# Kernel tuning notes

Hardware: AMD Instinct MI355X
Metric: run time of the kernel (lower is better)

## Reference

```python
import jax, jax.numpy as jnp
import numpy as np

DIM = 512
HEADS = 8
DEPTH = DIM // HEADS
DFF = 2048
EPS = 1e-3  # keras BatchNormalization default epsilon


def _dense_params(key, d_in, d_out, bias=True):
    k1, k2 = jax.random.split(key)
    lim = 1.0 / np.sqrt(d_in)
    W = jax.random.uniform(k1, (d_in, d_out), minval=-lim, maxval=lim, dtype=jnp.float32)
    if bias:
        b = jnp.zeros((d_out,), jnp.float32)
        return W, b
    return W


def _bn_params(key, d):
    k1, k2 = jax.random.split(key)
    gamma = 1.0 + 0.1 * jax.random.normal(k1, (d,), jnp.float32)
    beta = 0.1 * jax.random.normal(k2, (d,), jnp.float32)
    mean = 0.05 * jax.random.normal(jax.random.fold_in(key, 7), (d,), jnp.float32)
    var = jnp.ones((d,), jnp.float32)
    return gamma, beta, mean, var


def setup_inputs() -> dict:
    key = jax.random.key(0)
    ks = jax.random.split(key, 20)
    B, S_dec, S_enc = 32, 384, 384
    inp = {
        'enc_output': jax.random.normal(ks[0], (B, S_enc, DIM), jnp.float32),
        'x2': jax.random.normal(ks[1], (B, S_dec, DIM), jnp.float32),
    }
    # mha1 (self-attn) params
    for i, nm in enumerate(['q1', 'k1', 'v1', 'o1']):
        W, b = _dense_params(ks[2 + i], DIM, DIM)
        inp[f'W{nm}'], inp[f'b{nm}'] = W, b
    # mha2 (cross-attn) params
    for i, nm in enumerate(['q2', 'k2', 'v2', 'o2']):
        W, b = _dense_params(ks[6 + i], DIM, DIM)
        inp[f'W{nm}'], inp[f'b{nm}'] = W, b
    # FFN
    inp['Wff1'] = _dense_params(ks[10], DIM, DFF, bias=False)
    inp['Wff2'] = _dense_params(ks[11], DFF, DIM, bias=False)
    # 4 batchnorms
    for i in range(1, 5):
        g, be, m, v = _bn_params(ks[11 + i], DIM)
        inp[f'bn{i}_gamma'], inp[f'bn{i}_beta'] = g, be
        inp[f'bn{i}_mean'], inp[f'bn{i}_var'] = m, v
    return inp


def _split_heads(x):
    B, S, _ = x.shape
    return x.reshape(B, S, HEADS, DEPTH).transpose(0, 2, 1, 3)


def _mha(q_in, k_in, v_in, Wq, bq, Wk, bk, Wv, bv, Wo, bo, causal):
    q = _split_heads(q_in @ Wq + bq)
    k = _split_heads(k_in @ Wk + bk)
    v = _split_heads(v_in @ Wv + bv)
    logits = jnp.einsum('bhqd,bhkd->bhqk', q, k) / jnp.sqrt(jnp.float32(DEPTH))
    if causal:
        Sq, Sk = logits.shape[-2], logits.shape[-1]
        mask = jnp.tril(jnp.ones((Sq, Sk), bool))
        logits = jnp.where(mask, logits, jnp.finfo(logits.dtype).min)
    attn = jax.nn.softmax(logits, axis=-1)
    out = jnp.einsum('bhqk,bhkd->bhqd', attn, v)
    B, _, S, _ = out.shape
    out = out.transpose(0, 2, 1, 3).reshape(B, S, DIM)
    return out @ Wo + bo


def _bn(x, gamma, beta, mean, var):
    return (x - mean) * jax.lax.rsqrt(var + EPS) * gamma + beta


def reference(enc_output, x2,
              Wq1, bq1, Wk1, bk1, Wv1, bv1, Wo1, bo1,
              Wq2, bq2, Wk2, bk2, Wv2, bv2, Wo2, bo2,
              Wff1, Wff2,
              bn1_gamma, bn1_beta, bn1_mean, bn1_var,
              bn2_gamma, bn2_beta, bn2_mean, bn2_var,
              bn3_gamma, bn3_beta, bn3_mean, bn3_var,
              bn4_gamma, bn4_beta, bn4_mean, bn4_var):
    # self-attention with causal mask (dropout = identity)
    x = _mha(x2, x2, x2, Wq1, bq1, Wk1, bk1, Wv1, bv1, Wo1, bo1, causal=True)
    x = x + x2
    xn = _bn(x, bn1_gamma, bn1_beta, bn1_mean, bn1_var)
    y = _bn(enc_output, bn2_gamma, bn2_beta, bn2_mean, bn2_var)
    # cross-attention (no mask); residual adds x2 (as in source)
    x = _mha(xn, y, y, Wq2, bq2, Wk2, bk2, Wv2, bv2, Wo2, bo2, causal=False)
    x = x + x2
    cross_out = x
    x = _bn(x, bn3_gamma, bn3_beta, bn3_mean, bn3_var)
    x = jax.nn.relu(x @ Wff1) @ Wff2
    x = x + cross_out
    x = _bn(x, bn4_gamma, bn4_beta, bn4_mean, bn4_var)
    return x
```

## Files before the change

### kernel.cpp

```cpp
#include <hip/hip_runtime.h>
#include <cstdint>
#include <cstddef>

typedef __bf16 bf16;
typedef __bf16 bf16x8 __attribute__((ext_vector_type(8)));
typedef __bf16 bf16x4 __attribute__((ext_vector_type(4)));
typedef float  f32x4  __attribute__((ext_vector_type(4)));

#define B_   32
#define S_   384
#define D_   512
#define H_   8
#define DH_  64
#define DFF_ 2048
#define NTOK (B_*S_)

__device__ __forceinline__ void gload16(const void* g, void* l){
  __builtin_amdgcn_global_load_lds((__attribute__((address_space(1))) uint32_t*)(g),
                                   (__attribute__((address_space(3))) uint32_t*)(l), 16, 0, 0);
}

struct Ptr8 { const float* s[8]; };
__global__ __launch_bounds__(256) void transpose_w8(Ptr8 ps, bf16* dst){
  __shared__ float t[64][65];
  int w = blockIdx.z;
  const float* src = ps.s[w];
  bf16* d = dst + (size_t)w*512*512;
  int tr = blockIdx.y*64, tc = blockIdx.x*64;
  for (int i=threadIdx.x; i<4096; i+=256){ int r=i>>6, c=i&63; t[r][c] = src[(size_t)(tr+r)*512 + tc+c]; }
  __syncthreads();
  for (int i=threadIdx.x; i<4096; i+=256){ int c=i>>6, r=i&63; d[(size_t)(tc+c)*512 + tr+r] = (bf16)t[r][c]; }
}

__global__ __launch_bounds__(256) void transpose_rc(const float* __restrict__ src, bf16* __restrict__ dst,
                                                    int R, int C){
  __shared__ float t[64][65];
  int tr = blockIdx.y*64, tc = blockIdx.x*64;
  for (int i=threadIdx.x; i<4096; i+=256){ int r=i>>6, c=i&63; t[r][c] = src[(size_t)(tr+r)*C + tc+c]; }
  __syncthreads();
  for (int i=threadIdx.x; i<4096; i+=256){ int c=i>>6, r=i&63; dst[(size_t)(tc+c)*R + tr+r] = (bf16)t[r][c]; }
}

struct Ptr16 { const float* p[16]; };
__global__ __launch_bounds__(512) void bn_prep(Ptr16 q, float* sc, float* sh){
  int i = blockIdx.x;
  int n = threadIdx.x;
  float g = q.p[i*4+0][n];
  float b = q.p[i*4+1][n];
  float m = q.p[i*4+2][n];
  float v = q.p[i*4+3][n];
  float s = g * rsqrtf(v + 1e-3f);
  sc[i*512+n] = s;
  sh[i*512+n] = b - m*s;
}

__global__ __launch_bounds__(256) void cvt2(const float* __restrict__ enc, const float* __restrict__ x2,
                                            const float* __restrict__ sc, const float* __restrict__ sh,
                                            bf16* __restrict__ E2, bf16* __restrict__ X2b){
  size_t e0 = ((size_t)blockIdx.x*256 + threadIdx.x)*4;
  if (blockIdx.y == 0){
    int n0 = (int)(e0 & (D_-1));
    f32x4 xv = *(const f32x4*)(enc + e0);
    bf16x4 ov;
    #pragma unroll
    for (int j=0;j<4;j++) ov[j] = (bf16)(xv[j]*sc[n0+j] + sh[n0+j]);
    *(bf16x4*)(E2 + e0) = ov;
  } else {
    f32x4 xv = *(const f32x4*)(x2 + e0);
    bf16x4 ov;
    #pragma unroll
    for (int j=0;j<4;j++) ov[j] = (bf16)xv[j];
    *(bf16x4*)(X2b + e0) = ov;
  }
}

__global__ __launch_bounds__(256,3) void gemm_bt(
    const bf16* __restrict__ A, const bf16* __restrict__ Wt,
    const float* __restrict__ b0, const float* __restrict__ b1, const float* __restrict__ b2,
    const bf16* __restrict__ residb,
    const float* __restrict__ bsc, const float* __restrict__ bsh,
    bf16* __restrict__ o0, bf16* __restrict__ o1b,
    bf16* __restrict__ vt, int vseg,
    float* __restrict__ of, bf16* __restrict__ pre,
    int M, int N, int K, int relu, int mode)
{
  __shared__ bf16 As[2][64*64];
  __shared__ bf16 Bs[2][128*64];
  int nwg = gridDim.x;
  int cpx = nwg >> 3;
  int bid = blockIdx.x;
  int swz = (bid & 7)*cpx + (bid >> 3);
  int tiles_n = N >> 7;
  int tm = swz / tiles_n, tn = swz - tm*tiles_n;

  int tid = threadIdx.x, wave = tid>>6, lane = tid&63;
  int lhi = lane>>4, llo = lane&15;
  int lrow = lane>>3, lcol = lane&7;
  int wr = wave>>1, wc = wave&1;

  f32x4 acc[2][4];
  #pragma unroll
  for (int i=0;i<2;i++)
    #pragma unroll
    for (int j=0;j<4;j++) acc[i][j] = (f32x4){0.f,0.f,0.f,0.f};

  const bf16* Abase = A  + (size_t)(tm*64)  * K;
  const bf16* Bbase = Wt + (size_t)(tn*128) * K;

  int arow0 = wave*16, brow0 = wave*32;

  auto STAGE = [&](int buf, int kt){
    #pragma unroll
    for (int q=0;q<2;q++){
      int r = arow0 + q*8 + lrow;
      int s = lcol ^ (r&7);
      gload16(Abase + (size_t)r*K + kt + s*8, (char*)&As[buf][0] + wave*2048 + q*1024);
    }
    #pragma unroll
    for (int q=0;q<4;q++){
      int r = brow0 + q*8 + lrow;
      int s = lcol ^ (r&7);
      gload16(Bbase + (size_t)r*K + kt + s*8, (char*)&Bs[buf][0] + wave*4096 + q*1024);
    }
  };

  STAGE(0, 0);
  __syncthreads();
  int nt = K >> 6;
  int cur = 0;
  for (int t=0; t<nt; ++t){
    if (t+1 < nt) STAGE(cur^1, (t+1)<<6);
    #pragma unroll
    for (int ks=0; ks<2; ks++){
      bf16x8 af[2], bfr[4];
      #pragma unroll
      for (int i=0;i<2;i++){
        int row = wr*32 + i*16 + llo;
        int slot = (ks*4 + lhi) ^ (row&7);
        af[i] = *(const bf16x8*)&As[cur][row*64 + slot*8];
      }
      #pragma unroll
      for (int j=0;j<4;j++){
        int row = wc*64 + j*16 + llo;
        int slot = (ks*4 + lhi) ^ (row&7);
        bfr[j] = *(const bf16x8*)&Bs[cur][row*64 + slot*8];
      }
      #pragma unroll
      for (int i=0;i<2;i++)
        #pragma unroll
        for (int j=0;j<4;j++)
          acc[i][j] = __builtin_amdgcn_mfma_f32_16x16x32_bf16(af[i], bfr[j], acc[i][j], 0,0,0);
    }
    __syncthreads();
    cur ^= 1;
  }

  int m0 = tm*64 + wr*32, n0 = tn*128 + wc*64;
  #pragma unroll
  for (int i=0;i<2;i++){
    #pragma unroll
    for (int j=0;j<4;j++){
      int gn = n0 + j*16 + llo;
      float vv[4];
      #pragma unroll
      for (int rr=0;rr<4;rr++){
        int gm = m0 + i*16 + lhi*4 + rr;
        float v = acc[i][j][rr];
        if (b0){
          const float* bp = (gn < 512) ? b0 : ((gn < 1024) ? b1 : b2);
          v += bp[gn & 511];
        }
        if (residb) v += (float)residb[(size_t)gm*N + gn];
        vv[rr] = v;
      }
      int gm0 = m0 + i*16 + lhi*4;
      if (mode == 1){
        int seg = gn >> 9, cn = gn & 511;
        int h = cn >> 6, dd = cn & 63;
        int bb = gm0 / S_, ss0 = gm0 - bb*S_;
        if (seg == vseg){
          bf16x4 v4;
          #pragma unroll
          for (int rr=0;rr<4;rr++) v4[rr] = (bf16)vv[rr];
          *(bf16x4*)&vt[((size_t)(bb*H_ + h)*DH_ + dd)*S_ + ss0] = v4;
        } else {
          bf16* hp = (seg == 0) ? o0 : o1b;
          #pragma unroll
          for (int rr=0;rr<4;rr++)
            hp[(((size_t)(bb*H_ + h))*S_ + ss0 + rr)*DH_ + dd] = (bf16)vv[rr];
        }
      } else {
        #pragma unroll
        for (int rr=0;rr<4;rr++){
          int gm = gm0 + rr;
          float v = vv[rr];
          if (pre)  pre[(size_t)gm*N + gn] = (bf16)v;
          if (bsc)  v = v*bsc[gn & 511] + bsh[gn & 511];
          if (relu) v = fmaxf(v, 0.f);
          if (of) of[(size_t)gm*N + gn] = v;
          else    o0[(size_t)gm*N + gn] = (bf16)v;
        }
      }
    }
  }
}

__global__ __launch_bounds__(256,4) void gemm_bt2(
    const bf16* __restrict__ A, const bf16* __restrict__ Wt,
    const float* __restrict__ b0, const float* __restrict__ b1, const float* __restrict__ b2,
    const bf16* __restrict__ residb,
    bf16* __restrict__ o0, bf16* __restrict__ o1b,
    bf16* __restrict__ vt, int vseg,
    int M, int N, int K, int relu, int mode)
{
  __shared__ bf16 As[2][128*32];
  __shared__ bf16 Bs[2][128*32];
  int nwg = gridDim.x;
  int cpx = nwg >> 3;
  int bid = blockIdx.x;
  int swz = (bid & 7)*cpx + (bid >> 3);
  int tiles_n = N >> 7;
  int tm = swz / tiles_n, tn = swz - tm*tiles_n;

  int tid = threadIdx.x, wave = tid>>6, lane = tid&63;
  int lhi = lane>>4, llo = lane&15;
  int srow = lane>>2, sslot = lane&3;
  int wr = wave>>1, wc = wave&1;

  f32x4 acc[4][4];
  #pragma unroll
  for (int i=0;i<4;i++)
    #pragma unroll
    for (int j=0;j<4;j++) acc[i][j] = (f32x4){0.f,0.f,0.f,0.f};

  const bf16* Abase = A  + (size_t)(tm*128) * K;
  const bf16* Bbase = Wt + (size_t)(tn*128) * K;

  auto STAGE = [&](int buf, int kt){
    #pragma unroll
    for (int q=0;q<2;q++){
      int r = wave*32 + q*16 + srow;
      int s = sslot ^ ((r>>1)&3);
      gload16(Abase + (size_t)r*K + kt + s*8, (char*)&As[buf][0] + wave*2048 + q*1024);
    }
    #pragma unroll
    for (int q=0;q<2;q++){
      int r = wave*32 + q*16 + srow;
      int s = sslot ^ ((r>>1)&3);
      gload16(Bbase + (size_t)r*K + kt + s*8, (char*)&Bs[buf][0] + wave*2048 + q*1024);
    }
  };

  STAGE(0, 0);
  __syncthreads();
  int nt = K >> 5;
  int cur = 0;
  for (int t=0; t<nt; ++t){
    if (t+1 < nt) STAGE(cur^1, (t+1)<<5);
    bf16x8 af[4], bfr[4];
    #pragma unroll
    for (int i=0;i<4;i++){
      int row = wr*64 + i*16 + llo;
      int slot = lhi ^ ((row>>1)&3);
      af[i] = *(const bf16x8*)&As[cur][row*32 + slot*8];
    }
    #pragma unroll
    for (int j=0;j<4;j++){
      int row = wc*64 + j*16 + llo;
      int slot = lhi ^ ((row>>1)&3);
      bfr[j] = *(const bf16x8*)&Bs[cur][row*32 + slot*8];
    }
    #pragma unroll
    for (int i=0;i<4;i++)
      #pragma unroll
      for (int j=0;j<4;j++)
        acc[i][j] = __builtin_amdgcn_mfma_f32_16x16x32_bf16(af[i], bfr[j], acc[i][j], 0,0,0);
    __syncthreads();
    cur ^= 1;
  }

  int m0 = tm*128 + wr*64, n0 = tn*128 + wc*64;
  #pragma unroll
  for (int i=0;i<4;i++){
    #pragma unroll
    for (int j=0;j<4;j++){
      int gn = n0 + j*16 + llo;
      float vv[4];
      #pragma unroll
      for (int rr=0;rr<4;rr++){
        int gm = m0 + i*16 + lhi*4 + rr;
        float v = acc[i][j][rr];
        if (b0){
          const float* bp = (gn < 512) ? b0 : ((gn < 1024) ? b1 : b2);
          v += bp[gn & 511];
        }
        if (residb) v += (float)residb[(size_t)gm*N + gn];
        vv[rr] = v;
      }
      int gm0 = m0 + i*16 + lhi*4;
      if (mode == 1){
        int seg = gn >> 9, cn = gn & 511;
        int h = cn >> 6, dd = cn & 63;
        int bb = gm0 / S_, ss0 = gm0 - bb*S_;
        if (seg == vseg){
          bf16x4 v4;
          #pragma unroll
          for (int rr=0;rr<4;rr++) v4[rr] = (bf16)vv[rr];
          *(bf16x4*)&vt[((size_t)(bb*H_ + h)*DH_ + dd)*S_ + ss0] = v4;
        } else {
          bf16* hp = (seg == 0) ? o0 : o1b;
          #pragma unroll
          for (int rr=0;rr<4;rr++)
            hp[(((size_t)(bb*H_ + h))*S_ + ss0 + rr)*DH_ + dd] = (bf16)vv[rr];
        }
      } else {
        #pragma unroll
        for (int rr=0;rr<4;rr++){
          int gm = gm0 + rr;
          float v = vv[rr];
          if (relu) v = fmaxf(v, 0.f);
          o0[(size_t)gm*N + gn] = (bf16)v;
        }
      }
    }
  }
}

__global__ __launch_bounds__(256,4) void attn(
    const bf16* __restrict__ Q, const bf16* __restrict__ Kx,
    const bf16* __restrict__ Vt, bf16* __restrict__ out, int causal)
{
  __shared__ bf16 Ks[64*64];
  __shared__ bf16 Vs[64*64];
  __shared__ bf16 Ps[4][16*64];
  int bid = blockIdx.x;
  int bh = bid & 255;
  int qb = bid >> 8;
  int b = bh >> 3, h = bh & 7;
  int tid = threadIdx.x, wave = tid>>6, lane = tid&63;
  int lhi = lane>>4, llo = lane&15;
  int l7 = llo & 7;
  const bf16* Qb = Q  + (size_t)bh*S_*DH_;
  const bf16* Kb = Kx + (size_t)bh*S_*DH_;
  const bf16* Vb = Vt + (size_t)bh*DH_*S_;

  bf16x8 qf[2];
  #pragma unroll
  for (int f=0; f<2; f++)
    qf[f] = *(const bf16x8*)&Qb[(size_t)(qb*64 + wave*16 + llo)*DH_ + f*32 + lhi*8];

  f32x4 oacc[4];
  #pragma unroll
  for (int f=0; f<4; f++) oacc[f] = (f32x4){0.f,0.f,0.f,0.f};
  float mrow[4], lrow4[4];
  #pragma unroll
  for (int r=0;r<4;r++){ mrow[r] = -1e9f; lrow4[r] = 0.f; }

  int KT = causal ? (qb+1) : (S_/64);

  int srow0 = tid>>3, sslot = tid&7;
  bf16x8 kreg[2], vreg[2];

  auto issue = [&](int kb){
    const bf16* kt0 = Kb + (size_t)kb*64*DH_;
    #pragma unroll
    for (int s=0;s<2;s++){
      int row = s*32 + srow0;
      kreg[s] = *(const bf16x8*)&kt0[(size_t)row*64 + sslot*8];
      vreg[s] = *(const bf16x8*)&Vb[(size_t)row*S_ + (size_t)kb*64 + sslot*8];
    }
  };
  issue(0);

  for (int kb=0; kb<KT; kb++){
    #pragma unroll
    for (int s=0;s<2;s++){
      int row = s*32 + srow0;
      int sl = sslot ^ (row&7);
      *(bf16x8*)&Ks[row*64 + sl*8] = kreg[s];
      *(bf16x8*)&Vs[row*64 + sl*8] = vreg[s];
    }
    __syncthreads();

    f32x4 sc[4];
    #pragma unroll
    for (int f=0; f<4; f++){
      f32x4 z = (f32x4){0.f,0.f,0.f,0.f};
      #pragma unroll
      for (int ks=0; ks<2; ks++){
        int row = f*16 + llo;
        int slot = (ks*4 + lhi) ^ (row&7);
        bf16x8 kf = *(const bf16x8*)&Ks[row*64 + slot*8];
        z = __builtin_amdgcn_mfma_f32_16x16x32_bf16(qf[ks], kf, z, 0,0,0);
      }
      sc[f] = z;
    }
    #pragma unroll
    for (int f=0; f<4; f++)
      #pragma unroll
      for (int r=0;r<4;r++){
        float v = sc[f][r]*0.125f;
        if (causal && kb==KT-1){
          int gcol = kb*64 + f*16 + llo;
          int grow = qb*64 + wave*16 + lhi*4 + r;
          if (gcol > grow) v = -1e9f;
        }
        sc[f][r] = v;
      }

    float alpha[4], psum[4];
    #pragma unroll
    for (int r=0;r<4;r++){
      float vm = fmaxf(fmaxf(sc[0][r],sc[1][r]), fmaxf(sc[2][r],sc[3][r]));
      #pragma unroll
      for (int msk=1; msk<16; msk<<=1) vm = fmaxf(vm, __shfl_xor(vm, msk));
      float mn = fmaxf(mrow[r], vm);
      alpha[r] = __expf(mrow[r]-mn);
      mrow[r]  = mn;
      psum[r]  = 0.f;
    }
    #pragma unroll
    for (int f=0; f<4; f++)
      #pragma unroll
      for (int r=0;r<4;r++){
        float p = __expf(sc[f][r]-mrow[r]);
        psum[r] += p;
        int row = lhi*4 + r;
        int slot = (f*2 + (llo>>3)) ^ (row&7);
        Ps[wave][row*64 + slot*8 + l7] = (bf16)p;
      }
    #pragma unroll
    for (int r=0;r<4;r++){
      float s = psum[r];
      #pragma unroll
      for (int msk=1; msk<16; msk<<=1) s += __shfl_xor(s, msk);
      lrow4[r] = lrow4[r]*alpha[r] + s;
      #pragma unroll
      for (int f=0; f<4; f++) oacc[f][r] *= alpha[r];
    }

    if (kb+1 < KT) issue(kb+1);

    asm volatile("s_waitcnt lgkmcnt(0)" ::: "memory");
    __builtin_amdgcn_sched_barrier(0);

    #pragma unroll
    for (int ks=0; ks<2; ks++){
      int pslot = (ks*4 + lhi) ^ l7;
      bf16x8 pf = *(const bf16x8*)&Ps[wave][llo*64 + pslot*8];
      #pragma unroll
      for (int f2=0; f2<4; f2++){
        int row = f2*16 + llo;
        int slot = (ks*4 + lhi) ^ (row&7);
        bf16x8 vf = *(const bf16x8*)&Vs[row*64 + slot*8];
        oacc[f2] = __builtin_amdgcn_mfma_f32_16x16x32_bf16(pf, vf, oacc[f2], 0,0,0);
      }
    }
    __syncthreads();
  }

  int qg = qb*64 + wave*16;
  #pragma unroll
  for (int f2=0; f2<4; f2++)
    #pragma unroll
    for (int r=0;r<4;r++){
      int row = qg + lhi*4 + r;
      int dd  = f2*16 + llo;
      out[((size_t)(b*S_ + row))*D_ + h*DH_ + dd] = (bf16)(oacc[f2][r] / lrow4[r]);
    }
}

extern "C" void kernel_launch(void* const* d_in, const int* in_sizes, int n_in,
                              void* d_out, int out_size, void* d_ws, size_t ws_size,
                              hipStream_t stream)
{
  (void)in_sizes; (void)n_in; (void)out_size; (void)ws_size;
  const float* enc = (const float*)d_in[0];
  const float* x2  = (const float*)d_in[1];
  const float* Wq1 = (const float*)d_in[2];  const float* bq1 = (const float*)d_in[3];
  const float* Wk1 = (const float*)d_in[4];  const float* bk1 = (const float*)d_in[5];
  const float* Wv1 = (const float*)d_in[6];  const float* bv1 = (const float*)d_in[7];
  const float* Wo1 = (const float*)d_in[8];  const float* bo1 = (const float*)d_in[9];
  const float* Wq2 = (const float*)d_in[10]; const float* bq2 = (const float*)d_in[11];
  const float* Wk2 = (const float*)d_in[12]; const float* bk2 = (const float*)d_in[13];
  const float* Wv2 = (const float*)d_in[14]; const float* bv2 = (const float*)d_in[15];
  const float* Wo2 = (const float*)d_in[16]; const float* bo2 = (const float*)d_in[17];
  const float* Wff1= (const float*)d_in[18]; const float* Wff2= (const float*)d_in[19];
  float* outp = (float*)d_out;

  char* ws = (char*)d_ws;
  size_t off = 0;
  auto alloc = [&](size_t bytes)->void*{ void* p = ws + off; off += (bytes+255)&~(size_t)255; return p; };
  bf16* Wt8   = (bf16*)alloc((size_t)8*512*512*2);
  bf16* Wff1t = (bf16*)alloc((size_t)DFF_*D_*2);
  bf16* Wff2t = (bf16*)alloc((size_t)D_*DFF_*2);
  float* bnsc = (float*)alloc(4*512*4);
  float* bnsh = (float*)alloc(4*512*4);
  size_t actB = (size_t)NTOK*D_*2;
  bf16* X2b  = (bf16*)alloc(actB);
  bf16* Abuf = (bf16*)alloc(actB);
  bf16* Bbuf = (bf16*)alloc(actB);
  bf16* Cbuf = (bf16*)alloc(actB);
  bf16* Dv   = (bf16*)alloc(actB);
  bf16* E1   = (bf16*)alloc(actB);
  bf16* E2   = (bf16*)alloc(actB);
  bf16* E3   = E2;
  bf16* Fbuf = Abuf;

  bf16* Wtq1 = Wt8 + 0*262144;
  bf16* Wto1 = Wt8 + 3*262144;
  bf16* Wtq2 = Wt8 + 4*262144;
  bf16* Wtk2 = Wt8 + 5*262144;
  bf16* Wto2 = Wt8 + 7*262144;

  Ptr8 p8;
  p8.s[0]=Wq1; p8.s[1]=Wk1; p8.s[2]=Wv1; p8.s[3]=Wo1;
  p8.s[4]=Wq2; p8.s[5]=Wk2; p8.s[6]=Wv2; p8.s[7]=Wo2;
  transpose_w8<<<dim3(8,8,8),256,0,stream>>>(p8, Wt8);
  transpose_rc<<<dim3(DFF_/64, D_/64),256,0,stream>>>(Wff1, Wff1t, D_, DFF_);
  transpose_rc<<<dim3(D_/64, DFF_/64),256,0,stream>>>(Wff2, Wff2t, DFF_, D_);

  Ptr16 p16;
  for (int i=0;i<16;i++) p16.p[i] = (const float*)d_in[20+i];
  bn_prep<<<4,512,0,stream>>>(p16, bnsc, bnsh);
  cvt2<<<dim3(NTOK*D_/4/256, 2),256,0,stream>>>(enc, x2, bnsc+512, bnsh+512, E2, X2b);

  auto gemm = [&](const bf16* Am, const bf16* W,
                  const float* bb0, const float* bb1, const float* bb2,
                  const bf16* residb, const float* sc, const float* sh,
                  bf16* oo0, bf16* oo1, bf16* vt, int vseg,
                  float* of, bf16* pre,
                  int N, int K, int relu, int mode){
    gemm_bt<<<(NTOK/64)*(N/128), 256, 0, stream>>>(Am, W, bb0, bb1, bb2, residb, sc, sh,
                                                   oo0, oo1, vt, vseg, of, pre,
                                                   NTOK, N, K, relu, mode);
  };
  auto gemm2 = [&](const bf16* Am, const bf16* W,
                   const float* bb0, const float* bb1, const float* bb2,
                   bf16* oo0, bf16* oo1, bf16* vt, int vseg,
                   int N, int K, int relu, int mode){
    gemm_bt2<<<(NTOK/128)*(N/128), 256, 0, stream>>>(Am, W, bb0, bb1, bb2, nullptr,
                                                     oo0, oo1, vt, vseg,
                                                     NTOK, N, K, relu, mode);
  };

  gemm2(X2b, Wtq1, bq1, bk1, bv1, Abuf, Bbuf, Dv, 2, 1536, 512, 0, 1);
  attn<<<(S_/64)*B_*H_, 256, 0, stream>>>(Abuf, Bbuf, Dv, Cbuf, 1);
  gemm(Cbuf, Wto1, bo1, nullptr, nullptr, X2b, bnsc+0, bnsh+0,
       E1, nullptr, nullptr, -1, nullptr, nullptr, 512, 512, 0, 0);

  gemm(E1, Wtq2, bq2, nullptr, nullptr, nullptr, nullptr, nullptr,
       Abuf, nullptr, nullptr, -1, nullptr, nullptr, 512, 512, 0, 1);
  gemm2(E2, Wtk2, bk2, bv2, nullptr, Bbuf, nullptr, Dv, 1, 1024, 512, 0, 1);
  attn<<<(S_/64)*B_*H_, 256, 0, stream>>>(Abuf, Bbuf, Dv, Cbuf, 0);
  gemm(Cbuf, Wto2, bo2, nullptr, nullptr, X2b, bnsc+2*512, bnsh+2*512,
       E1, nullptr, nullptr, -1, nullptr, E3, 512, 512, 0, 0);

  gemm2(E1, Wff1t, nullptr, nullptr, nullptr, Fbuf, nullptr, nullptr, -1, DFF_, 512, 1, 0);
  gemm(Fbuf, Wff2t, nullptr, nullptr, nullptr, E3, bnsc+3*512, bnsh+3*512,
       nullptr, nullptr, nullptr, -1, outp, nullptr, 512, DFF_, 0, 0);
}
```

Before: 316.3 us.

## Double-buffer attention K/V tiles and merge weight prep kernels into one launch

The attention kernel now keeps two LDS buffers for K and V and prefetches two tiles ahead in registers. The next tile is written to the other buffer after the PV MMAs, which drops the trailing barrier per iteration. Separately, the weight transposes and batchnorm folding are merged into a single launch, removing three kernel launches. The extra LDS (16KB more per block) may reduce occupancy of the attention kernel, which has launch_bounds(256,4).

```diff
diff --git a/kernel.cpp b/kernel.cpp
--- a/kernel.cpp
+++ b/kernel.cpp
@@ -20,38 +20,37 @@
                                    (__attribute__((address_space(3))) uint32_t*)(l), 16, 0, 0);
 }
 
-struct Ptr8 { const float* s[8]; };
-__global__ __launch_bounds__(256) void transpose_w8(Ptr8 ps, bf16* dst){
+struct PrepArgs { const float* w8[8]; const float* wff1; const float* wff2; const float* bn[16]; };
+__global__ __launch_bounds__(256) void prep_all(PrepArgs pa, bf16* Wt8, bf16* Wff1t, bf16* Wff2t,
+                                                float* sc, float* sh){
   __shared__ float t[64][65];
-  int w = blockIdx.z;
-  const float* src = ps.s[w];
-  bf16* d = dst + (size_t)w*512*512;
-  int tr = blockIdx.y*64, tc = blockIdx.x*64;
-  for (int i=threadIdx.x; i<4096; i+=256){ int r=i>>6, c=i&63; t[r][c] = src[(size_t)(tr+r)*512 + tc+c]; }
-  __syncthreads();
-  for (int i=threadIdx.x; i<4096; i+=256){ int c=i>>6, r=i&63; d[(size_t)(tc+c)*512 + tr+r] = (bf16)t[r][c]; }
-}
-
-__global__ __launch_bounds__(256) void transpose_rc(const float* __restrict__ src, bf16* __restrict__ dst,
-                                                    int R, int C){
-  __shared__ float t[64][65];
-  int tr = blockIdx.y*64, tc = blockIdx.x*64;
-  for (int i=threadIdx.x; i<4096; i+=256){ int r=i>>6, c=i&63; t[r][c] = src[(size_t)(tr+r)*C + tc+c]; }
-  __syncthreads();
-  for (int i=threadIdx.x; i<4096; i+=256){ int c=i>>6, r=i&63; dst[(size_t)(tc+c)*R + tr+r] = (bf16)t[r][c]; }
-}
-
-struct Ptr16 { const float* p[16]; };
-__global__ __launch_bounds__(512) void bn_prep(Ptr16 q, float* sc, float* sh){
-  int i = blockIdx.x;
-  int n = threadIdx.x;
-  float g = q.p[i*4+0][n];
-  float b = q.p[i*4+1][n];
-  float m = q.p[i*4+2][n];
-  float v = q.p[i*4+3][n];
-  float s = g * rsqrtf(v + 1e-3f);
-  sc[i*512+n] = s;
-  sh[i*512+n] = b - m*s;
+  int id = blockIdx.x;
+  if (id < 1024){
+    const float* src; bf16* dst; int R, C, tr, tc;
+    if (id < 512){
+      int w = id >> 6, tl = id & 63;
+      src = pa.w8[w]; dst = Wt8 + (size_t)w*262144; R = 512; C = 512;
+      tr = (tl>>3)*64; tc = (tl&7)*64;
+    } else if (id < 768){
+      int tl = id - 512;
+      src = pa.wff1; dst = Wff1t; R = 512; C = 2048;
+      tr = (tl>>5)*64; tc = (tl&31)*64;
+    } else {
+      int tl = id - 768;
+      src = pa.wff2; dst = Wff2t; R = 2048; C = 512;
+      tr = (tl>>3)*64; tc = (tl&7)*64;
+    }
+    for (int i=threadIdx.x; i<4096; i+=256){ int r=i>>6, c=i&63; t[r][c] = src[(size_t)(tr+r)*C + tc+c]; }
+    __syncthreads();
+    for (int i=threadIdx.x; i<4096; i+=256){ int c=i>>6, r=i&63; dst[(size_t)(tc+c)*R + tr+r] = (bf16)t[r][c]; }
+  } else {
+    int t2 = id - 1024;
+    int i = t2 >> 1, half = t2 & 1;
+    int n = half*256 + threadIdx.x;
+    float g = pa.bn[i*4+0][n], b = pa.bn[i*4+1][n], m = pa.bn[i*4+2][n], v = pa.bn[i*4+3][n];
+    float s = g * rsqrtf(v + 1e-3f);
+    sc[i*512+n] = s; sh[i*512+n] = b - m*s;
+  }
 }
 
 __global__ __launch_bounds__(256) void cvt2(const float* __restrict__ enc, const float* __restrict__ x2,
@@ -330,8 +329,8 @@
     const bf16* __restrict__ Q, const bf16* __restrict__ Kx,
     const bf16* __restrict__ Vt, bf16* __restrict__ out, int causal)
 {
-  __shared__ bf16 Ks[64*64];
-  __shared__ bf16 Vs[64*64];
+  __shared__ bf16 Ks[2][64*64];
+  __shared__ bf16 Vs[2][64*64];
   __shared__ bf16 Ps[4][16*64];
   int bid = blockIdx.x;
   int bh = bid & 255;
@@ -359,27 +358,33 @@
   int KT = causal ? (qb+1) : (S_/64);
 
   int srow0 = tid>>3, sslot = tid&7;
-  bf16x8 kreg[2], vreg[2];
-
-  auto issue = [&](int kb){
+  bf16x8 krA[2], vrA[2], krB[2], vrB[2];
+
+  auto ISSUE = [&](bf16x8 (&KR)[2], bf16x8 (&VR)[2], int kb){
     const bf16* kt0 = Kb + (size_t)kb*64*DH_;
     #pragma unroll
     for (int s=0;s<2;s++){
       int row = s*32 + srow0;
-      kreg[s] = *(const bf16x8*)&kt0[(size_t)row*64 + sslot*8];
-      vreg[s] = *(const bf16x8*)&Vb[(size_t)row*S_ + (size_t)kb*64 + sslot*8];
+      KR[s] = *(const bf16x8*)&kt0[(size_t)row*64 + sslot*8];
+      VR[s] = *(const bf16x8*)&Vb[(size_t)row*S_ + (size_t)kb*64 + sslot*8];
     }
   };
-  issue(0);
-
-  for (int kb=0; kb<KT; kb++){
+  auto COMMIT = [&](bf16x8 (&KR)[2], bf16x8 (&VR)[2], int buf){
     #pragma unroll
     for (int s=0;s<2;s++){
       int row = s*32 + srow0;
       int sl = sslot ^ (row&7);
-      *(bf16x8*)&Ks[row*64 + sl*8] = kreg[s];
-      *(bf16x8*)&Vs[row*64 + sl*8] = vreg[s];
-    }
+      *(bf16x8*)&Ks[buf][row*64 + sl*8] = KR[s];
+      *(bf16x8*)&Vs[buf][row*64 + sl*8] = VR[s];
+    }
+  };
+
+  ISSUE(krA, vrA, 0);
+  COMMIT(krA, vrA, 0);
+  if (KT > 1) ISSUE(krB, vrB, 1);
+
+  for (int kb=0; kb<KT; kb++){
+    int buf = kb & 1;
     __syncthreads();
 
     f32x4 sc[4];
@@ -390,7 +395,7 @@
       for (int ks=0; ks<2; ks++){
         int row = f*16 + llo;
         int slot = (ks*4 + lhi) ^ (row&7);
-        bf16x8 kf = *(const bf16x8*)&Ks[row*64 + slot*8];
+        bf16x8 kf = *(const bf16x8*)&Ks[buf][row*64 + slot*8];
         z = __builtin_amdgcn_mfma_f32_16x16x32_bf16(qf[ks], kf, z, 0,0,0);
       }
       sc[f] = z;
@@ -439,7 +444,10 @@
       for (int f=0; f<4; f++) oacc[f][r] *= alpha[r];
     }
 
-    if (kb+1 < KT) issue(kb+1);
+    if (kb+2 < KT){
+      if ((kb & 1) == 0) ISSUE(krA, vrA, kb+2);
+      else               ISSUE(krB, vrB, kb+2);
+    }
 
     asm volatile("s_waitcnt lgkmcnt(0)" ::: "memory");
     __builtin_amdgcn_sched_barrier(0);
@@ -452,11 +460,15 @@
       for (int f2=0; f2<4; f2++){
         int row = f2*16 + llo;
         int slot = (ks*4 + lhi) ^ (row&7);
-        bf16x8 vf = *(const bf16x8*)&Vs[row*64 + slot*8];
+        bf16x8 vf = *(const bf16x8*)&Vs[buf][row*64 + slot*8];
         oacc[f2] = __builtin_amdgcn_mfma_f32_16x16x32_bf16(pf, vf, oacc[f2], 0,0,0);
       }
     }
-    __syncthreads();
+
+    if (kb+1 < KT){
+      if ((kb & 1) == 0) COMMIT(krB, vrB, buf^1);
+      else               COMMIT(krA, vrA, buf^1);
+    }
   }
 
   int qg = qb*64 + wave*16;
@@ -477,15 +489,14 @@
   (void)in_sizes; (void)n_in; (void)out_size; (void)ws_size;
   const float* enc = (const float*)d_in[0];
   const float* x2  = (const float*)d_in[1];
-  const float* Wq1 = (const float*)d_in[2];  const float* bq1 = (const float*)d_in[3];
-  const float* Wk1 = (const float*)d_in[4];  const float* bk1 = (const float*)d_in[5];
-  const float* Wv1 = (const float*)d_in[6];  const float* bv1 = (const float*)d_in[7];
-  const float* Wo1 = (const float*)d_in[8];  const float* bo1 = (const float*)d_in[9];
-  const float* Wq2 = (const float*)d_in[10]; const float* bq2 = (const float*)d_in[11];
-  const float* Wk2 = (const float*)d_in[12]; const float* bk2 = (const float*)d_in[13];
-  const float* Wv2 = (const float*)d_in[14]; const float* bv2 = (const float*)d_in[15];
-  const float* Wo2 = (const float*)d_in[16]; const float* bo2 = (const float*)d_in[17];
-  const float* Wff1= (const float*)d_in[18]; const float* Wff2= (const float*)d_in[19];
+  const float* bq1 = (const float*)d_in[3];
+  const float* bk1 = (const float*)d_in[5];
+  const float* bv1 = (const float*)d_in[7];
+  const float* bo1 = (const float*)d_in[9];
+  const float* bq2 = (const float*)d_in[11];
+  const float* bk2 = (const float*)d_in[13];
+  const float* bv2 = (const float*)d_in[15];
+  const float* bo2 = (const float*)d_in[17];
   float* outp = (float*)d_out;
 
   char* ws = (char*)d_ws;
@@ -513,16 +524,14 @@
   bf16* Wtk2 = Wt8 + 5*262144;
   bf16* Wto2 = Wt8 + 7*262144;
 
-  Ptr8 p8;
-  p8.s[0]=Wq1; p8.s[1]=Wk1; p8.s[2]=Wv1; p8.s[3]=Wo1;
-  p8.s[4]=Wq2; p8.s[5]=Wk2; p8.s[6]=Wv2; p8.s[7]=Wo2;
-  transpose_w8<<<dim3(8,8,8),256,0,stream>>>(p8, Wt8);
-  transpose_rc<<<dim3(DFF_/64, D_/64),256,0,stream>>>(Wff1, Wff1t, D_, DFF_);
-  transpose_rc<<<dim3(D_/64, DFF_/64),256,0,stream>>>(Wff2, Wff2t, DFF_, D_);
-
-  Ptr16 p16;
-  for (int i=0;i<16;i++) p16.p[i] = (const float*)d_in[20+i];
-  bn_prep<<<4,512,0,stream>>>(p16, bnsc, bnsh);
+  PrepArgs pa;
+  pa.w8[0]=(const float*)d_in[2];  pa.w8[1]=(const float*)d_in[4];
+  pa.w8[2]=(const float*)d_in[6];  pa.w8[3]=(const float*)d_in[8];
+  pa.w8[4]=(const float*)d_in[10]; pa.w8[5]=(const float*)d_in[12];
+  pa.w8[6]=(const float*)d_in[14]; pa.w8[7]=(const float*)d_in[16];
+  pa.wff1=(const float*)d_in[18];  pa.wff2=(const float*)d_in[19];
+  for (int i=0;i<16;i++) pa.bn[i] = (const float*)d_in[20+i];
+  prep_all<<<1032,256,0,stream>>>(pa, Wt8, Wff1t, Wff2t, bnsc, bnsh);
   cvt2<<<dim3(NTOK*D_/4/256, 2),256,0,stream>>>(enc, x2, bnsc+512, bnsh+512, E2, X2b);
 
   auto gemm = [&](const bf16* Am, const bf16* W,
```

Result: slower. 327.4 us (+3.5%).
